# Kernel tuning notes

Hardware: AMD Instinct MI355X
Metric: run time of the kernel (lower is better)

The kernel has to match this reference:

```python
import jax, jax.numpy as jnp
import numpy as np

D_MODEL = 1024
H = 16
D_V = 64
B = 4
N = 1024
LARGE_NEG = -1000000000.0


def setup_inputs() -> dict:
    key = jax.random.key(0)
    k_x, k_q, k_k, k_v, k_o = jax.random.split(key, 5)
    X = jax.random.normal(k_x, (B, N, D_MODEL), dtype=jnp.float32)
    W_q = jax.random.normal(k_q, (H, D_MODEL, D_MODEL), dtype=jnp.float32)
    W_k = jax.random.normal(k_k, (H, D_MODEL, D_MODEL), dtype=jnp.float32)
    W_v = jax.random.normal(k_v, (H, D_MODEL, D_V), dtype=jnp.float32)
    W_o = jax.random.normal(k_o, (H * D_V, D_MODEL), dtype=jnp.float32)
    return {"X": X, "W_q": W_q, "W_k": W_k, "W_v": W_v, "W_o": W_o}


def reference(X, W_q, W_k, W_v, W_o):
    Bb, Nn, Dd = X.shape
    scale = 1.0 / jnp.sqrt(jnp.asarray(Dd, dtype=X.dtype))
    # Per-head projections, batched over heads instead of a Python loop.
    Q = jnp.einsum('bnd,hde->bhne', X, W_q)          # [B,H,N,d_model]
    K = jnp.einsum('bnd,hde->bhne', X, W_k)          # [B,H,N,d_model]
    V = jnp.einsum('bnd,hdv->bhnv', X, W_v)          # [B,H,N,D_v]
    scores = jnp.einsum('bhne,bhme->bhnm', Q, K) * scale  # [B,H,N,N]
    A = jax.nn.softmax(scores, axis=-1)
    Hh = jnp.einsum('bhnm,bhmv->bhnv', A, V)         # [B,H,N,D_v]
    concat = Hh.transpose(0, 2, 1, 3).reshape(Bb, Nn, -1)  # [B,N,H*D_v]
    Y = concat @ W_o                                  # [B,N,d_model]
    # Post-hoc mask: triu over the LAST TWO dims (N, d_model), diagonal=1.
    mask = jnp.triu(jnp.ones((Nn, Dd), dtype=bool), k=1)
    return jnp.where(mask[None, :, :], jnp.asarray(LARGE_NEG, Y.dtype), Y)
```

## Files before the change

kernel.cpp:

```cpp
#include <hip/hip_runtime.h>
#include <stdint.h>

typedef short s16x8 __attribute__((ext_vector_type(8)));
typedef float f32x4 __attribute__((ext_vector_type(4)));

__device__ __forceinline__ unsigned short f2bf(float f) {
  union { float f; unsigned int u; } v; v.f = f;
  unsigned int r = v.u + 0x7FFFu + ((v.u >> 16) & 1u);
  return (unsigned short)(r >> 16);
}

__device__ __forceinline__ unsigned cvt2fp8(float a, float b) {
#if __has_builtin(__builtin_amdgcn_cvt_pk_fp8_f32)
  return (unsigned)__builtin_amdgcn_cvt_pk_fp8_f32(a, b, 0, false);
#else
  unsigned r;
  asm("v_cvt_pk_fp8_f32 %0, %1, %2" : "=v"(r) : "v"(a), "v"(b));
  return r;
#endif
}

__device__ __forceinline__ void gload_lds16(const void* g, void* l) {
  __builtin_amdgcn_global_load_lds(
      (const __attribute__((address_space(1))) unsigned int*)g,
      (__attribute__((address_space(3))) unsigned int*)l, 16, 0, 0);
}

__device__ __forceinline__ unsigned xcd_swz(unsigned fid, unsigned nwg) {
  unsigned cpx = nwg >> 3;
  return (fid & 7) * cpx + (fid >> 3);
}

__global__ void conv_bf16(const float* __restrict__ in, unsigned short* __restrict__ out, int n8) {
  int i = blockIdx.x * blockDim.x + threadIdx.x;
  if (i >= n8) return;
  const f32x4* p = (const f32x4*)(in + (long)i * 8);
  f32x4 a = p[0], b = p[1];
  s16x8 o;
  o[0]=(short)f2bf(a[0]); o[1]=(short)f2bf(a[1]); o[2]=(short)f2bf(a[2]); o[3]=(short)f2bf(a[3]);
  o[4]=(short)f2bf(b[0]); o[5]=(short)f2bf(b[1]); o[6]=(short)f2bf(b[2]); o[7]=(short)f2bf(b[3]);
  *(s16x8*)(out + (long)i * 8) = o;
}

__global__ void conv_x(const float* __restrict__ in, unsigned short* __restrict__ obf,
                       unsigned char* __restrict__ of8, int n8) {
  int i = blockIdx.x * blockDim.x + threadIdx.x;
  if (i >= n8) return;
  const f32x4* p = (const f32x4*)(in + (long)i * 8);
  f32x4 a = p[0], b = p[1];
  s16x8 o;
  o[0]=(short)f2bf(a[0]); o[1]=(short)f2bf(a[1]); o[2]=(short)f2bf(a[2]); o[3]=(short)f2bf(a[3]);
  o[4]=(short)f2bf(b[0]); o[5]=(short)f2bf(b[1]); o[6]=(short)f2bf(b[2]); o[7]=(short)f2bf(b[3]);
  *(s16x8*)(obf + (long)i * 8) = o;
  unsigned long w = (unsigned long)(cvt2fp8(a[0], a[1]) & 0xFFFFu)
                  | ((unsigned long)(cvt2fp8(a[2], a[3]) & 0xFFFFu) << 16)
                  | ((unsigned long)(cvt2fp8(b[0], b[1]) & 0xFFFFu) << 32)
                  | ((unsigned long)(cvt2fp8(b[2], b[3]) & 0xFFFFu) << 48);
  *(unsigned long*)(of8 + (long)i * 8) = w;
}

__global__ void convT_wv(const float* __restrict__ in, unsigned short* __restrict__ out) {
  int i = blockIdx.x * blockDim.x + threadIdx.x;
  int v = i & 63, d = (i >> 6) & 1023, h = i >> 16;
  out[((long)h * 64 + v) * 1024 + d] = f2bf(in[i]);
}

__global__ void convT_wo(const float* __restrict__ in, unsigned short* __restrict__ out) {
  int i = blockIdx.x * blockDim.x + threadIdx.x;
  int e = i & 1023, c = i >> 10;
  out[(long)e * 1024 + c] = f2bf(in[i]);
}

template<int BM, int BN, int WAVES_M, int WAVES_N, int CMODE>
__global__ __launch_bounds__(256, 2)
void gemm_bt(const unsigned short* __restrict__ A, const unsigned short* __restrict__ BT,
             void* __restrict__ Cout, int aDiv, long aStr, int bMod, long bStr,
             long cStr, int ldc)
{
  constexpr int BK = 64;
  constexpr int FM = BM / (WAVES_M * 16);
  constexpr int FN = BN / (WAVES_N * 16);
  __shared__ __align__(16) unsigned short At[BM * BK];
  __shared__ __align__(16) unsigned short Bt[BN * BK];

  unsigned fid = blockIdx.x + gridDim.x * (blockIdx.y + gridDim.y * blockIdx.z);
  unsigned nwg = gridDim.x * gridDim.y * gridDim.z;
  unsigned sid = xcd_swz(fid, nwg);
  unsigned bx = sid % gridDim.x;
  unsigned rem = sid / gridDim.x;
  unsigned by = rem % gridDim.y;
  unsigned bz = rem / gridDim.y;

  const int t = threadIdx.x;
  const int l = t & 63;
  const int g = l >> 4, c = l & 15;
  const int w = t >> 6;
  const int wr = (w / WAVES_N) * (BM / WAVES_M);
  const int wc = (w % WAVES_N) * (BN / WAVES_N);
  const int z = bz;
  const int m0 = by * BM;
  const int n0 = bx * BN;
  const unsigned short* Ab = A + (long)(z / aDiv) * aStr + (long)m0 * 1024;
  const unsigned short* Bb = BT + (long)(z % bMod) * bStr + (long)n0 * 1024;

  const long cbase = (long)z * cStr;

  if constexpr (CMODE == 2) {
    if (n0 > m0 + BM - 1) {
#pragma unroll
      for (int m = 0; m < FM; ++m)
#pragma unroll
        for (int n = 0; n < FN; ++n)
#pragma unroll
          for (int r = 0; r < 4; ++r) {
            int row = wr + m * 16 + g * 4 + r;
            int col = n0 + wc + n * 16 + c;
            ((float*)Cout)[cbase + (long)(m0 + row) * ldc + col] = -1e9f;
          }
      return;
    }
  }

  f32x4 acc[FM][FN] = {};
  constexpr int PA = (BM * BK) / 2048;
  constexpr int PB = (BN * BK) / 2048;

  for (int k0 = 0; k0 < 1024; k0 += BK) {
#pragma unroll
    for (int p = 0; p < PA; ++p) {
      int e = (p * 256 + t) * 8;
      int row = e >> 6, col = e & 63;
      gload_lds16(Ab + (long)row * 1024 + k0 + col, &At[e]);
    }
#pragma unroll
    for (int p = 0; p < PB; ++p) {
      int e = (p * 256 + t) * 8;
      int row = e >> 6, col = e & 63;
      gload_lds16(Bb + (long)row * 1024 + k0 + col, &Bt[e]);
    }
    __syncthreads();
#pragma unroll
    for (int kk = 0; kk < BK; kk += 32) {
      s16x8 af[FM], bf[FN];
#pragma unroll
      for (int m = 0; m < FM; ++m)
        af[m] = *(const s16x8*)&At[(wr + m * 16 + c) * BK + kk + g * 8];
#pragma unroll
      for (int n = 0; n < FN; ++n)
        bf[n] = *(const s16x8*)&Bt[(wc + n * 16 + c) * BK + kk + g * 8];
#pragma unroll
      for (int m = 0; m < FM; ++m)
#pragma unroll
        for (int n = 0; n < FN; ++n)
          acc[m][n] = __builtin_amdgcn_mfma_f32_16x16x32_bf16(af[m], bf[n], acc[m][n], 0, 0, 0);
    }
    __syncthreads();
  }

#pragma unroll
  for (int m = 0; m < FM; ++m)
#pragma unroll
    for (int n = 0; n < FN; ++n) {
      if constexpr (CMODE == 3) {
        int row0 = m0 + wr + m * 16 + g * 4;
        int col  = n0 + wc + n * 16 + c;
        unsigned p01 = cvt2fp8(acc[m][n][0] * 0.00390625f, acc[m][n][1] * 0.00390625f);
        unsigned p23 = cvt2fp8(acc[m][n][2] * 0.00390625f, acc[m][n][3] * 0.00390625f);
        unsigned char* Cp = (unsigned char*)Cout + cbase + (long)row0 * ldc + col;
        Cp[0]            = (unsigned char)p01;
        Cp[(long)ldc]    = (unsigned char)(p01 >> 8);
        Cp[(long)ldc*2]  = (unsigned char)p23;
        Cp[(long)ldc*3]  = (unsigned char)(p23 >> 8);
      } else {
#pragma unroll
        for (int r = 0; r < 4; ++r) {
          int row = wr + m * 16 + g * 4 + r;
          int col = n0 + wc + n * 16 + c;
          int grow = m0 + row;
          float v = acc[m][n][r];
          if constexpr (CMODE == 0) {
            ((unsigned short*)Cout)[cbase + (long)grow * ldc + col] = f2bf(v);
          } else if constexpr (CMODE == 1) {
            ((unsigned short*)Cout)[cbase + (long)col * ldc + grow] = f2bf(v);
          } else if constexpr (CMODE == 2) {
            ((float*)Cout)[cbase + (long)grow * ldc + col] = (col > grow) ? -1e9f : v;
          }
        }
      }
    }
}

__global__ __launch_bounds__(256, 2)
void gemm_f8(const unsigned char* __restrict__ A, const unsigned char* __restrict__ BT,
             unsigned char* __restrict__ Cout)
{
  __shared__ __align__(16) unsigned char At[128 * 128];
  __shared__ __align__(16) unsigned char Bt[128 * 128];

  unsigned fid = blockIdx.x + gridDim.x * (blockIdx.y + gridDim.y * blockIdx.z);
  unsigned nwg = gridDim.x * gridDim.y * gridDim.z;
  unsigned sid = xcd_swz(fid, nwg);
  unsigned bx = sid % gridDim.x;
  unsigned rem = sid / gridDim.x;
  unsigned by = rem % gridDim.y;
  unsigned bz = rem / gridDim.y;

  const int t = threadIdx.x;
  const int l = t & 63;
  const int g = l >> 4, c = l & 15;
  const int w = t >> 6;
  const int wr = (w >> 1) * 64;
  const int wc = (w & 1) * 64;
  const int z = bz;
  const int m0 = by * 128;
  const int n0 = bx * 128;
  const unsigned char* Ab = A + (long)(z >> 4) * (1 << 20) + (long)m0 * 1024;
  const unsigned char* Bb = BT + (long)(z & 15) * (1 << 20) + (long)n0 * 1024;

  f32x4 acc[4][4] = {};

  for (int k0 = 0; k0 < 1024; k0 += 128) {
#pragma unroll
    for (int p = 0; p < 4; ++p) {
      int e = (p * 256 + t) * 16;
      int r = e >> 7, u = (e >> 4) & 7;
      int gcol = ((u ^ (r & 7)) << 4);
      gload_lds16(Ab + (long)r * 1024 + k0 + gcol, &At[e]);
    }
#pragma unroll
    for (int p = 0; p < 4; ++p) {
      int e = (p * 256 + t) * 16;
      int r = e >> 7, u = (e >> 4) & 7;
      int gcol = ((u ^ (r & 7)) << 4);
      gload_lds16(Bb + (long)r * 1024 + k0 + gcol, &Bt[e]);
    }
    __syncthreads();
#pragma unroll
    for (int kk = 0; kk < 128; kk += 32) {
      long af[4], bf[4];
#pragma unroll
      for (int m = 0; m < 4; ++m) {
        int row = wr + m * 16 + c;
        int un = (kk >> 4) + (g >> 1);
        af[m] = *(const long*)&At[row * 128 + ((un ^ (row & 7)) << 4) + (g & 1) * 8];
      }
#pragma unroll
      for (int n = 0; n < 4; ++n) {
        int row = wc + n * 16 + c;
        int un = (kk >> 4) + (g >> 1);
        bf[n] = *(const long*)&Bt[row * 128 + ((un ^ (row & 7)) << 4) + (g & 1) * 8];
      }
      __builtin_amdgcn_s_setprio(1);
#pragma unroll
      for (int m = 0; m < 4; ++m)
#pragma unroll
        for (int n = 0; n < 4; ++n)
          acc[m][n] = __builtin_amdgcn_mfma_f32_16x16x32_fp8_fp8(af[m], bf[n], acc[m][n], 0, 0, 0);
      __builtin_amdgcn_s_setprio(0);
    }
    __syncthreads();
  }

  const long cbase = (long)z << 20;
#pragma unroll
  for (int m = 0; m < 4; ++m)
#pragma unroll
    for (int n = 0; n < 4; ++n) {
      int row0 = m0 + wr + m * 16 + g * 4;
      int col  = n0 + wc + n * 16 + c;
      unsigned p01 = cvt2fp8(acc[m][n][0], acc[m][n][1]);
      unsigned p23 = cvt2fp8(acc[m][n][2], acc[m][n][3]);
      unsigned char* Cp = Cout + cbase + (long)row0 * 1024 + col;
      Cp[0]    = (unsigned char)p01;
      Cp[1024] = (unsigned char)(p01 >> 8);
      Cp[2048] = (unsigned char)p23;
      Cp[3072] = (unsigned char)(p23 >> 8);
    }
}

__global__ __launch_bounds__(256, 2)
void flash_attn(const unsigned char* __restrict__ T, const unsigned char* __restrict__ X,
                const unsigned short* __restrict__ VT, unsigned short* __restrict__ Yc)
{
  __shared__ __align__(16) unsigned char Sh[49152];
  unsigned char* Tt = Sh;
  unsigned char* Xt = Sh + 16384;
  unsigned short* Vt = (unsigned short*)(Sh + 32768);
  unsigned short* Pl = (unsigned short*)Sh;

  unsigned fid = blockIdx.x + gridDim.x * blockIdx.y;
  unsigned nwg = gridDim.x * gridDim.y;
  unsigned sid = xcd_swz(fid, nwg);
  const int q0 = (sid % gridDim.x) * 128;
  const int bh = sid / gridDim.x;

  const int t = threadIdx.x;
  const int l = t & 63;
  const int w = t >> 6;
  const int g = l >> 4;
  const int c = l & 15;
  const int b = bh >> 4;

  const unsigned char* Tq = T + (long)bh * (1024 * 1024) + (long)q0 * 1024;
  const unsigned char* Xb = X + (long)b * (1024 * 1024);
  const unsigned short* Vb = VT + (long)bh * (64 * 1024);

  f32x4 accO[2][4] = {};
  float mrun[2][4], lrun[2][4];
#pragma unroll
  for (int m = 0; m < 2; ++m)
#pragma unroll
    for (int r = 0; r < 4; ++r) { mrun[m][r] = -1e30f; lrun[m][r] = 0.f; }

  const float scale = 8.0f;

  for (int m0 = 0; m0 < 1024; m0 += 128) {
    f32x4 accS[2][8] = {};
    for (int k0 = 0; k0 < 1024; k0 += 128) {
#pragma unroll
      for (int p = 0; p < 4; ++p) {
        int e = (p * 256 + t) * 16;
        int r = e >> 7, u = (e >> 4) & 7;
        int gcol = ((u ^ (r & 7)) << 4);
        gload_lds16(Tq + (long)r * 1024 + k0 + gcol, &Tt[e]);
      }
#pragma unroll
      for (int p = 0; p < 4; ++p) {
        int e = (p * 256 + t) * 16;
        int r = e >> 7, u = (e >> 4) & 7;
        int gcol = ((u ^ (r & 7)) << 4);
        gload_lds16(Xb + (long)(m0 + r) * 1024 + k0 + gcol, &Xt[e]);
      }
      __syncthreads();
#pragma unroll
      for (int kk = 0; kk < 128; kk += 32) {
        long af[2], bf[8];
#pragma unroll
        for (int m = 0; m < 2; ++m) {
          int row = w * 32 + m * 16 + c;
          int un = (kk >> 4) + (g >> 1);
          af[m] = *(const long*)&Tt[row * 128 + ((un ^ (row & 7)) << 4) + (g & 1) * 8];
        }
#pragma unroll
        for (int n = 0; n < 8; ++n) {
          int row = n * 16 + c;
          int un = (kk >> 4) + (g >> 1);
          bf[n] = *(const long*)&Xt[row * 128 + ((un ^ (row & 7)) << 4) + (g & 1) * 8];
        }
        __builtin_amdgcn_s_setprio(1);
#pragma unroll
        for (int m = 0; m < 2; ++m)
#pragma unroll
          for (int n = 0; n < 8; ++n)
            accS[m][n] = __builtin_amdgcn_mfma_f32_16x16x32_fp8_fp8(af[m], bf[n], accS[m][n], 0, 0, 0);
        __builtin_amdgcn_s_setprio(0);
      }
      __syncthreads();
    }
#pragma unroll
    for (int p = 0; p < 4; ++p) {
      int e = (p * 256 + t) * 8;
      int r = e >> 7, u = (e >> 3) & 15;
      int gcol = ((u ^ (r & 7)) << 3);
      gload_lds16(Vb + (long)r * 1024 + m0 + gcol, &Vt[e]);
    }
    float alpha[2][4];
#pragma unroll
    for (int m = 0; m < 2; ++m) {
#pragma unroll
      for (int r = 0; r < 4; ++r) {
        float mx = -1e30f;
#pragma unroll
        for (int n = 0; n < 8; ++n) mx = fmaxf(mx, accS[m][n][r]);
#pragma unroll
        for (int s = 1; s < 16; s <<= 1) mx = fmaxf(mx, __shfl_xor(mx, s));
        mx *= scale;
        float mnew = fmaxf(mrun[m][r], mx);
        float a = __expf(mrun[m][r] - mnew);
        alpha[m][r] = a;
        float sum = 0.f;
#pragma unroll
        for (int n = 0; n < 8; ++n) {
          float pe = __expf(accS[m][n][r] * scale - mnew);
          accS[m][n][r] = pe;
          sum += pe;
        }
#pragma unroll
        for (int s = 1; s < 16; s <<= 1) sum += __shfl_xor(sum, s);
        lrun[m][r] = lrun[m][r] * a + sum;
        mrun[m][r] = mnew;
      }
    }
#pragma unroll
    for (int m = 0; m < 2; ++m)
#pragma unroll
      for (int n = 0; n < 8; ++n)
#pragma unroll
        for (int r = 0; r < 4; ++r) {
          int row = w * 32 + m * 16 + g * 4 + r;
          int un = 2 * n + (c >> 3);
          Pl[row * 128 + ((un ^ (row & 7)) << 3) + (c & 7)] = f2bf(accS[m][n][r]);
        }
    __syncthreads();
#pragma unroll
    for (int m = 0; m < 2; ++m)
#pragma unroll
      for (int n = 0; n < 4; ++n)
#pragma unroll
        for (int r = 0; r < 4; ++r)
          accO[m][n][r] *= alpha[m][r];
#pragma unroll
    for (int kk = 0; kk < 128; kk += 32) {
      s16x8 pa[2], vb[4];
#pragma unroll
      for (int m = 0; m < 2; ++m) {
        int row = w * 32 + m * 16 + c;
        int un = (kk >> 3) + g;
        pa[m] = *(const s16x8*)&Pl[row * 128 + ((un ^ (row & 7)) << 3)];
      }
#pragma unroll
      for (int n = 0; n < 4; ++n) {
        int row = n * 16 + c;
        int un = (kk >> 3) + g;
        vb[n] = *(const s16x8*)&Vt[row * 128 + ((un ^ (row & 7)) << 3)];
      }
      __builtin_amdgcn_s_setprio(1);
#pragma unroll
      for (int m = 0; m < 2; ++m)
#pragma unroll
        for (int n = 0; n < 4; ++n)
          accO[m][n] = __builtin_amdgcn_mfma_f32_16x16x32_bf16(pa[m], vb[n], accO[m][n], 0, 0, 0);
      __builtin_amdgcn_s_setprio(0);
    }
    __syncthreads();
  }
  unsigned short* out = Yc + (long)b * (1024 * 1024) + (long)(bh & 15) * 64;
#pragma unroll
  for (int m = 0; m < 2; ++m)
#pragma unroll
    for (int n = 0; n < 4; ++n)
#pragma unroll
      for (int r = 0; r < 4; ++r) {
        int row = q0 + w * 32 + m * 16 + g * 4 + r;
        int col = n * 16 + c;
        out[(long)row * 1024 + col] = f2bf(accO[m][n][r] / lrun[m][r]);
      }
}

extern "C" void kernel_launch(void* const* d_in, const int* in_sizes, int n_in,
                              void* d_out, int out_size, void* d_ws, size_t ws_size,
                              hipStream_t stream) {
  (void)in_sizes; (void)n_in; (void)out_size; (void)ws_size;
  const float* X  = (const float*)d_in[0];
  const float* Wq = (const float*)d_in[1];
  const float* Wk = (const float*)d_in[2];
  const float* Wv = (const float*)d_in[3];
  const float* Wo = (const float*)d_in[4];
  float* Y = (float*)d_out;
  char* ws = (char*)d_ws;

  const long MB = 1L << 20;
  unsigned short* Xbf  = (unsigned short*)(ws + 0);
  unsigned short* Wqb  = (unsigned short*)(ws + 8  * MB);
  unsigned short* Wkb  = (unsigned short*)(ws + 40 * MB);
  unsigned char*  Mtf8 = (unsigned char*)(ws + 72 * MB);
  unsigned char*  Tf8  = (unsigned char*)(ws + 104 * MB);
  unsigned char*  Xf8  = (unsigned char*)(ws + 168 * MB);
  unsigned short* WvT  = (unsigned short*)(ws + 8  * MB);
  unsigned short* VTb  = (unsigned short*)(ws + 10 * MB);
  unsigned short* Ccat = (unsigned short*)(ws + 18 * MB);
  unsigned short* WoT  = (unsigned short*)(ws + 26 * MB);

  const long M1 = 1L << 20;

  conv_x   <<<2048, 256, 0, stream>>>(X,  Xbf, Xf8, 524288);
  conv_bf16<<<8192, 256, 0, stream>>>(Wq, Wqb, 2097152);
  conv_bf16<<<8192, 256, 0, stream>>>(Wk, Wkb, 2097152);

  gemm_bt<128, 128, 2, 2, 3><<<dim3(8, 8, 16), 256, 0, stream>>>(
      Wkb, Wqb, Mtf8, 1, M1, 16, M1, M1, 1024);

  gemm_f8<<<dim3(8, 8, 64), 256, 0, stream>>>(Xf8, Mtf8, Tf8);

  convT_wv<<<4096, 256, 0, stream>>>(Wv, WvT);
  gemm_bt<128, 64, 4, 1, 1><<<dim3(1, 8, 64), 256, 0, stream>>>(
      Xbf, WvT, VTb, 16, M1, 16, 65536, 65536, 1024);

  flash_attn<<<dim3(8, 64), 256, 0, stream>>>(Tf8, Xf8, VTb, Ccat);

  convT_wo<<<4096, 256, 0, stream>>>(Wo, WoT);
  gemm_bt<128, 128, 2, 2, 2><<<dim3(8, 8, 4), 256, 0, stream>>>(
      Ccat, WoT, Y, 1, M1, 1, 0, M1, 1024);
}
```

Measured before the change: 389.5 us.

## Double-buffer LDS tiles in fp8 GEMM and flash-attention score loops

Both the fp8 projection GEMM and the QK score loop in flash attention now use two LDS stages. The global-to-LDS loads for the next k-tile are issued before the MFMA work on the current tile, with explicit vmcnt waits and raw s_barrier calls in place of __syncthreads. The aim is to hide global load latency behind compute instead of stalling at each tile. In exchange, LDS per block grows to 64KB for the GEMM and 80KB for attention, which at two blocks per CU may limit occupancy.

Measured after the change: 403.6 us. +3.6%, slower.

```diff
diff --git a/kernel.cpp b/kernel.cpp
--- a/kernel.cpp
+++ b/kernel.cpp
@@ -194,8 +194,7 @@
 void gemm_f8(const unsigned char* __restrict__ A, const unsigned char* __restrict__ BT,
              unsigned char* __restrict__ Cout)
 {
-  __shared__ __align__(16) unsigned char At[128 * 128];
-  __shared__ __align__(16) unsigned char Bt[128 * 128];
+  __shared__ __align__(16) unsigned char Sh[65536];
 
   unsigned fid = blockIdx.x + gridDim.x * (blockIdx.y + gridDim.y * blockIdx.z);
   unsigned nwg = gridDim.x * gridDim.y * gridDim.z;
@@ -219,22 +218,51 @@
 
   f32x4 acc[4][4] = {};
 
-  for (int k0 = 0; k0 < 1024; k0 += 128) {
-#pragma unroll
-    for (int p = 0; p < 4; ++p) {
-      int e = (p * 256 + t) * 16;
-      int r = e >> 7, u = (e >> 4) & 7;
-      int gcol = ((u ^ (r & 7)) << 4);
-      gload_lds16(Ab + (long)r * 1024 + k0 + gcol, &At[e]);
-    }
-#pragma unroll
-    for (int p = 0; p < 4; ++p) {
-      int e = (p * 256 + t) * 16;
-      int r = e >> 7, u = (e >> 4) & 7;
-      int gcol = ((u ^ (r & 7)) << 4);
-      gload_lds16(Bb + (long)r * 1024 + k0 + gcol, &Bt[e]);
-    }
-    __syncthreads();
+#pragma unroll
+  for (int p = 0; p < 4; ++p) {
+    int e = (p * 256 + t) * 16;
+    int r = e >> 7, u = (e >> 4) & 7;
+    int gcol = ((u ^ (r & 7)) << 4);
+    gload_lds16(Ab + (long)r * 1024 + 0 + gcol, &Sh[e]);
+  }
+#pragma unroll
+  for (int p = 0; p < 4; ++p) {
+    int e = (p * 256 + t) * 16;
+    int r = e >> 7, u = (e >> 4) & 7;
+    int gcol = ((u ^ (r & 7)) << 4);
+    gload_lds16(Bb + (long)r * 1024 + 0 + gcol, &Sh[16384 + e]);
+  }
+
+  int cur = 0;
+  for (int it = 0; it < 8; ++it) {
+    int k0 = it << 7;
+    if (it < 7) {
+      unsigned char* Ad = Sh + (cur ^ 1) * 32768;
+      unsigned char* Bd = Ad + 16384;
+#pragma unroll
+      for (int p = 0; p < 4; ++p) {
+        int e = (p * 256 + t) * 16;
+        int r = e >> 7, u = (e >> 4) & 7;
+        int gcol = ((u ^ (r & 7)) << 4);
+        gload_lds16(Ab + (long)r * 1024 + (k0 + 128) + gcol, &Ad[e]);
+      }
+#pragma unroll
+      for (int p = 0; p < 4; ++p) {
+        int e = (p * 256 + t) * 16;
+        int r = e >> 7, u = (e >> 4) & 7;
+        int gcol = ((u ^ (r & 7)) << 4);
+        gload_lds16(Bb + (long)r * 1024 + (k0 + 128) + gcol, &Bd[e]);
+      }
+      asm volatile("s_waitcnt vmcnt(8)" ::: "memory");
+    } else {
+      asm volatile("s_waitcnt vmcnt(0)" ::: "memory");
+    }
+    __builtin_amdgcn_sched_barrier(0);
+    __builtin_amdgcn_s_barrier();
+    __builtin_amdgcn_sched_barrier(0);
+
+    const unsigned char* At = Sh + cur * 32768;
+    const unsigned char* Bt = At + 16384;
 #pragma unroll
     for (int kk = 0; kk < 128; kk += 32) {
       long af[4], bf[4];
@@ -258,7 +286,10 @@
           acc[m][n] = __builtin_amdgcn_mfma_f32_16x16x32_fp8_fp8(af[m], bf[n], acc[m][n], 0, 0, 0);
       __builtin_amdgcn_s_setprio(0);
     }
-    __syncthreads();
+    __builtin_amdgcn_sched_barrier(0);
+    __builtin_amdgcn_s_barrier();
+    __builtin_amdgcn_sched_barrier(0);
+    cur ^= 1;
   }
 
   const long cbase = (long)z << 20;
@@ -282,10 +313,8 @@
 void flash_attn(const unsigned char* __restrict__ T, const unsigned char* __restrict__ X,
                 const unsigned short* __restrict__ VT, unsigned short* __restrict__ Yc)
 {
-  __shared__ __align__(16) unsigned char Sh[49152];
-  unsigned char* Tt = Sh;
-  unsigned char* Xt = Sh + 16384;
-  unsigned short* Vt = (unsigned short*)(Sh + 32768);
+  __shared__ __align__(16) unsigned char Sh[81920];
+  unsigned short* Vt = (unsigned short*)(Sh + 65536);
   unsigned short* Pl = (unsigned short*)Sh;
 
   unsigned fid = blockIdx.x + gridDim.x * blockIdx.y;
@@ -316,22 +345,50 @@
 
   for (int m0 = 0; m0 < 1024; m0 += 128) {
     f32x4 accS[2][8] = {};
-    for (int k0 = 0; k0 < 1024; k0 += 128) {
-#pragma unroll
-      for (int p = 0; p < 4; ++p) {
-        int e = (p * 256 + t) * 16;
-        int r = e >> 7, u = (e >> 4) & 7;
-        int gcol = ((u ^ (r & 7)) << 4);
-        gload_lds16(Tq + (long)r * 1024 + k0 + gcol, &Tt[e]);
-      }
-#pragma unroll
-      for (int p = 0; p < 4; ++p) {
-        int e = (p * 256 + t) * 16;
-        int r = e >> 7, u = (e >> 4) & 7;
-        int gcol = ((u ^ (r & 7)) << 4);
-        gload_lds16(Xb + (long)(m0 + r) * 1024 + k0 + gcol, &Xt[e]);
-      }
-      __syncthreads();
+#pragma unroll
+    for (int p = 0; p < 4; ++p) {
+      int e = (p * 256 + t) * 16;
+      int r = e >> 7, u = (e >> 4) & 7;
+      int gcol = ((u ^ (r & 7)) << 4);
+      gload_lds16(Tq + (long)r * 1024 + 0 + gcol, &Sh[e]);
+    }
+#pragma unroll
+    for (int p = 0; p < 4; ++p) {
+      int e = (p * 256 + t) * 16;
+      int r = e >> 7, u = (e >> 4) & 7;
+      int gcol = ((u ^ (r & 7)) << 4);
+      gload_lds16(Xb + (long)(m0 + r) * 1024 + 0 + gcol, &Sh[16384 + e]);
+    }
+    int cur = 0;
+    for (int it = 0; it < 8; ++it) {
+      int k0 = it << 7;
+      if (it < 7) {
+        unsigned char* Td = Sh + (cur ^ 1) * 32768;
+        unsigned char* Xd = Td + 16384;
+#pragma unroll
+        for (int p = 0; p < 4; ++p) {
+          int e = (p * 256 + t) * 16;
+          int r = e >> 7, u = (e >> 4) & 7;
+          int gcol = ((u ^ (r & 7)) << 4);
+          gload_lds16(Tq + (long)r * 1024 + (k0 + 128) + gcol, &Td[e]);
+        }
+#pragma unroll
+        for (int p = 0; p < 4; ++p) {
+          int e = (p * 256 + t) * 16;
+          int r = e >> 7, u = (e >> 4) & 7;
+          int gcol = ((u ^ (r & 7)) << 4);
+          gload_lds16(Xb + (long)(m0 + r) * 1024 + (k0 + 128) + gcol, &Xd[e]);
+        }
+        asm volatile("s_waitcnt vmcnt(8)" ::: "memory");
+      } else {
+        asm volatile("s_waitcnt vmcnt(0)" ::: "memory");
+      }
+      __builtin_amdgcn_sched_barrier(0);
+      __builtin_amdgcn_s_barrier();
+      __builtin_amdgcn_sched_barrier(0);
+
+      const unsigned char* Tt = Sh + cur * 32768;
+      const unsigned char* Xt = Tt + 16384;
 #pragma unroll
       for (int kk = 0; kk < 128; kk += 32) {
         long af[2], bf[8];
@@ -355,7 +412,10 @@
             accS[m][n] = __builtin_amdgcn_mfma_f32_16x16x32_fp8_fp8(af[m], bf[n], accS[m][n], 0, 0, 0);
         __builtin_amdgcn_s_setprio(0);
       }
-      __syncthreads();
+      __builtin_amdgcn_sched_barrier(0);
+      __builtin_amdgcn_s_barrier();
+      __builtin_amdgcn_sched_barrier(0);
+      cur ^= 1;
     }
 #pragma unroll
     for (int p = 0; p < 4; ++p) {
```

## Move Wk·Wq, V projection and PV matmul from bf16 to fp8

Applied to the files above, without the earlier changes.

Converts Wq, Wk, Wv and X to fp8 only, dropping the bf16 copies. The Wk·Wq product and the V projection now run through a generalized templated fp8 GEMM, and the V projection output is stored transposed. Inside flash attention, P and V are kept as fp8 in LDS and the PV product uses the fp8 MFMA. The aim is to halve conversion and weight traffic and use the faster fp8 MFMA, at the cost of more precision loss in the weights, V and probabilities.

Result: faster. 346.6 us (-11.0%).

```diff
diff --git a/kernel.cpp b/kernel.cpp
--- a/kernel.cpp
+++ b/kernel.cpp
@@ -31,38 +31,22 @@
   return (fid & 7) * cpx + (fid >> 3);
 }
 
-__global__ void conv_bf16(const float* __restrict__ in, unsigned short* __restrict__ out, int n8) {
+__global__ void conv_fp8(const float* __restrict__ in, unsigned char* __restrict__ out, int n8) {
   int i = blockIdx.x * blockDim.x + threadIdx.x;
   if (i >= n8) return;
   const f32x4* p = (const f32x4*)(in + (long)i * 8);
   f32x4 a = p[0], b = p[1];
-  s16x8 o;
-  o[0]=(short)f2bf(a[0]); o[1]=(short)f2bf(a[1]); o[2]=(short)f2bf(a[2]); o[3]=(short)f2bf(a[3]);
-  o[4]=(short)f2bf(b[0]); o[5]=(short)f2bf(b[1]); o[6]=(short)f2bf(b[2]); o[7]=(short)f2bf(b[3]);
-  *(s16x8*)(out + (long)i * 8) = o;
-}
-
-__global__ void conv_x(const float* __restrict__ in, unsigned short* __restrict__ obf,
-                       unsigned char* __restrict__ of8, int n8) {
-  int i = blockIdx.x * blockDim.x + threadIdx.x;
-  if (i >= n8) return;
-  const f32x4* p = (const f32x4*)(in + (long)i * 8);
-  f32x4 a = p[0], b = p[1];
-  s16x8 o;
-  o[0]=(short)f2bf(a[0]); o[1]=(short)f2bf(a[1]); o[2]=(short)f2bf(a[2]); o[3]=(short)f2bf(a[3]);
-  o[4]=(short)f2bf(b[0]); o[5]=(short)f2bf(b[1]); o[6]=(short)f2bf(b[2]); o[7]=(short)f2bf(b[3]);
-  *(s16x8*)(obf + (long)i * 8) = o;
   unsigned long w = (unsigned long)(cvt2fp8(a[0], a[1]) & 0xFFFFu)
                   | ((unsigned long)(cvt2fp8(a[2], a[3]) & 0xFFFFu) << 16)
                   | ((unsigned long)(cvt2fp8(b[0], b[1]) & 0xFFFFu) << 32)
                   | ((unsigned long)(cvt2fp8(b[2], b[3]) & 0xFFFFu) << 48);
-  *(unsigned long*)(of8 + (long)i * 8) = w;
-}
-
-__global__ void convT_wv(const float* __restrict__ in, unsigned short* __restrict__ out) {
+  *(unsigned long*)(out + (long)i * 8) = w;
+}
+
+__global__ void convT_wv_f8(const float* __restrict__ in, unsigned char* __restrict__ out) {
   int i = blockIdx.x * blockDim.x + threadIdx.x;
   int v = i & 63, d = (i >> 6) & 1023, h = i >> 16;
-  out[((long)h * 64 + v) * 1024 + d] = f2bf(in[i]);
+  out[((long)h * 64 + v) * 1024 + d] = (unsigned char)cvt2fp8(in[i], 0.f);
 }
 
 __global__ void convT_wo(const float* __restrict__ in, unsigned short* __restrict__ out) {
@@ -160,42 +144,31 @@
 #pragma unroll
   for (int m = 0; m < FM; ++m)
 #pragma unroll
-    for (int n = 0; n < FN; ++n) {
-      if constexpr (CMODE == 3) {
-        int row0 = m0 + wr + m * 16 + g * 4;
-        int col  = n0 + wc + n * 16 + c;
-        unsigned p01 = cvt2fp8(acc[m][n][0] * 0.00390625f, acc[m][n][1] * 0.00390625f);
-        unsigned p23 = cvt2fp8(acc[m][n][2] * 0.00390625f, acc[m][n][3] * 0.00390625f);
-        unsigned char* Cp = (unsigned char*)Cout + cbase + (long)row0 * ldc + col;
-        Cp[0]            = (unsigned char)p01;
-        Cp[(long)ldc]    = (unsigned char)(p01 >> 8);
-        Cp[(long)ldc*2]  = (unsigned char)p23;
-        Cp[(long)ldc*3]  = (unsigned char)(p23 >> 8);
-      } else {
-#pragma unroll
-        for (int r = 0; r < 4; ++r) {
-          int row = wr + m * 16 + g * 4 + r;
-          int col = n0 + wc + n * 16 + c;
-          int grow = m0 + row;
-          float v = acc[m][n][r];
-          if constexpr (CMODE == 0) {
-            ((unsigned short*)Cout)[cbase + (long)grow * ldc + col] = f2bf(v);
-          } else if constexpr (CMODE == 1) {
-            ((unsigned short*)Cout)[cbase + (long)col * ldc + grow] = f2bf(v);
-          } else if constexpr (CMODE == 2) {
-            ((float*)Cout)[cbase + (long)grow * ldc + col] = (col > grow) ? -1e9f : v;
-          }
+    for (int n = 0; n < FN; ++n)
+#pragma unroll
+      for (int r = 0; r < 4; ++r) {
+        int row = wr + m * 16 + g * 4 + r;
+        int col = n0 + wc + n * 16 + c;
+        int grow = m0 + row;
+        float v = acc[m][n][r];
+        if constexpr (CMODE == 0) {
+          ((unsigned short*)Cout)[cbase + (long)grow * ldc + col] = f2bf(v);
+        } else if constexpr (CMODE == 2) {
+          ((float*)Cout)[cbase + (long)grow * ldc + col] = (col > grow) ? -1e9f : v;
         }
       }
-    }
-}
-
+}
+
+template<int BM, int BN, int WM, int WN, int TRANS>
 __global__ __launch_bounds__(256, 2)
 void gemm_f8(const unsigned char* __restrict__ A, const unsigned char* __restrict__ BT,
-             unsigned char* __restrict__ Cout)
+             unsigned char* __restrict__ Cout, int aDiv, long aStr, int bMod, long bStr,
+             long cStr, int ldc, float scale)
 {
-  __shared__ __align__(16) unsigned char At[128 * 128];
-  __shared__ __align__(16) unsigned char Bt[128 * 128];
+  constexpr int FM = BM / (WM * 16);
+  constexpr int FN = BN / (WN * 16);
+  __shared__ __align__(16) unsigned char At[BM * 128];
+  __shared__ __align__(16) unsigned char Bt[BN * 128];
 
   unsigned fid = blockIdx.x + gridDim.x * (blockIdx.y + gridDim.y * blockIdx.z);
   unsigned nwg = gridDim.x * gridDim.y * gridDim.z;
@@ -209,26 +182,28 @@
   const int l = t & 63;
   const int g = l >> 4, c = l & 15;
   const int w = t >> 6;
-  const int wr = (w >> 1) * 64;
-  const int wc = (w & 1) * 64;
+  const int wr = (w / WN) * (BM / WM);
+  const int wc = (w % WN) * (BN / WN);
   const int z = bz;
-  const int m0 = by * 128;
-  const int n0 = bx * 128;
-  const unsigned char* Ab = A + (long)(z >> 4) * (1 << 20) + (long)m0 * 1024;
-  const unsigned char* Bb = BT + (long)(z & 15) * (1 << 20) + (long)n0 * 1024;
-
-  f32x4 acc[4][4] = {};
+  const int m0 = by * BM;
+  const int n0 = bx * BN;
+  const unsigned char* Ab = A + (long)(z / aDiv) * aStr + (long)m0 * 1024;
+  const unsigned char* Bb = BT + (long)(z % bMod) * bStr + (long)n0 * 1024;
+
+  f32x4 acc[FM][FN] = {};
+  constexpr int PA = (BM * 128) / (256 * 16);
+  constexpr int PB = (BN * 128) / (256 * 16);
 
   for (int k0 = 0; k0 < 1024; k0 += 128) {
 #pragma unroll
-    for (int p = 0; p < 4; ++p) {
+    for (int p = 0; p < PA; ++p) {
       int e = (p * 256 + t) * 16;
       int r = e >> 7, u = (e >> 4) & 7;
       int gcol = ((u ^ (r & 7)) << 4);
       gload_lds16(Ab + (long)r * 1024 + k0 + gcol, &At[e]);
     }
 #pragma unroll
-    for (int p = 0; p < 4; ++p) {
+    for (int p = 0; p < PB; ++p) {
       int e = (p * 256 + t) * 16;
       int r = e >> 7, u = (e >> 4) & 7;
       int gcol = ((u ^ (r & 7)) << 4);
@@ -237,56 +212,61 @@
     __syncthreads();
 #pragma unroll
     for (int kk = 0; kk < 128; kk += 32) {
-      long af[4], bf[4];
-#pragma unroll
-      for (int m = 0; m < 4; ++m) {
+      long af[FM], bf[FN];
+#pragma unroll
+      for (int m = 0; m < FM; ++m) {
         int row = wr + m * 16 + c;
         int un = (kk >> 4) + (g >> 1);
         af[m] = *(const long*)&At[row * 128 + ((un ^ (row & 7)) << 4) + (g & 1) * 8];
       }
 #pragma unroll
-      for (int n = 0; n < 4; ++n) {
+      for (int n = 0; n < FN; ++n) {
         int row = wc + n * 16 + c;
         int un = (kk >> 4) + (g >> 1);
         bf[n] = *(const long*)&Bt[row * 128 + ((un ^ (row & 7)) << 4) + (g & 1) * 8];
       }
       __builtin_amdgcn_s_setprio(1);
 #pragma unroll
-      for (int m = 0; m < 4; ++m)
-#pragma unroll
-        for (int n = 0; n < 4; ++n)
+      for (int m = 0; m < FM; ++m)
+#pragma unroll
+        for (int n = 0; n < FN; ++n)
           acc[m][n] = __builtin_amdgcn_mfma_f32_16x16x32_fp8_fp8(af[m], bf[n], acc[m][n], 0, 0, 0);
       __builtin_amdgcn_s_setprio(0);
     }
     __syncthreads();
   }
 
-  const long cbase = (long)z << 20;
-#pragma unroll
-  for (int m = 0; m < 4; ++m)
-#pragma unroll
-    for (int n = 0; n < 4; ++n) {
+  const long cbase = (long)z * cStr;
+#pragma unroll
+  for (int m = 0; m < FM; ++m)
+#pragma unroll
+    for (int n = 0; n < FN; ++n) {
       int row0 = m0 + wr + m * 16 + g * 4;
       int col  = n0 + wc + n * 16 + c;
-      unsigned p01 = cvt2fp8(acc[m][n][0], acc[m][n][1]);
-      unsigned p23 = cvt2fp8(acc[m][n][2], acc[m][n][3]);
-      unsigned char* Cp = Cout + cbase + (long)row0 * 1024 + col;
-      Cp[0]    = (unsigned char)p01;
-      Cp[1024] = (unsigned char)(p01 >> 8);
-      Cp[2048] = (unsigned char)p23;
-      Cp[3072] = (unsigned char)(p23 >> 8);
+      unsigned p01 = cvt2fp8(acc[m][n][0] * scale, acc[m][n][1] * scale);
+      unsigned p23 = cvt2fp8(acc[m][n][2] * scale, acc[m][n][3] * scale);
+      if constexpr (TRANS == 0) {
+        unsigned char* Cp = Cout + cbase + (long)row0 * ldc + col;
+        Cp[0]            = (unsigned char)p01;
+        Cp[(long)ldc]    = (unsigned char)(p01 >> 8);
+        Cp[(long)ldc*2]  = (unsigned char)p23;
+        Cp[(long)ldc*3]  = (unsigned char)(p23 >> 8);
+      } else {
+        unsigned word = (p01 & 0xFFFFu) | (p23 << 16);
+        *(unsigned*)(Cout + cbase + (long)col * ldc + row0) = word;
+      }
     }
 }
 
 __global__ __launch_bounds__(256, 2)
 void flash_attn(const unsigned char* __restrict__ T, const unsigned char* __restrict__ X,
-                const unsigned short* __restrict__ VT, unsigned short* __restrict__ Yc)
+                const unsigned char* __restrict__ VT, unsigned short* __restrict__ Yc)
 {
-  __shared__ __align__(16) unsigned char Sh[49152];
-  unsigned char* Tt = Sh;
-  unsigned char* Xt = Sh + 16384;
-  unsigned short* Vt = (unsigned short*)(Sh + 32768);
-  unsigned short* Pl = (unsigned short*)Sh;
+  __shared__ __align__(16) unsigned char Sh[40960];
+  unsigned char* Tt  = Sh;
+  unsigned char* Xt  = Sh + 16384;
+  unsigned char* Vt8 = Sh + 32768;
+  unsigned char* Pl8 = Sh;
 
   unsigned fid = blockIdx.x + gridDim.x * blockIdx.y;
   unsigned nwg = gridDim.x * gridDim.y;
@@ -303,7 +283,7 @@
 
   const unsigned char* Tq = T + (long)bh * (1024 * 1024) + (long)q0 * 1024;
   const unsigned char* Xb = X + (long)b * (1024 * 1024);
-  const unsigned short* Vb = VT + (long)bh * (64 * 1024);
+  const unsigned char* Vb = VT + (long)bh * (64 * 1024);
 
   f32x4 accO[2][4] = {};
   float mrun[2][4], lrun[2][4];
@@ -358,11 +338,11 @@
       __syncthreads();
     }
 #pragma unroll
-    for (int p = 0; p < 4; ++p) {
-      int e = (p * 256 + t) * 8;
-      int r = e >> 7, u = (e >> 3) & 15;
-      int gcol = ((u ^ (r & 7)) << 3);
-      gload_lds16(Vb + (long)r * 1024 + m0 + gcol, &Vt[e]);
+    for (int p = 0; p < 2; ++p) {
+      int e = (p * 256 + t) * 16;
+      int r = e >> 7, u = (e >> 4) & 7;
+      int gcol = ((u ^ (r & 7)) << 4);
+      gload_lds16(Vb + (long)r * 1024 + m0 + gcol, &Vt8[e]);
     }
     float alpha[2][4];
 #pragma unroll
@@ -398,8 +378,8 @@
 #pragma unroll
         for (int r = 0; r < 4; ++r) {
           int row = w * 32 + m * 16 + g * 4 + r;
-          int un = 2 * n + (c >> 3);
-          Pl[row * 128 + ((un ^ (row & 7)) << 3) + (c & 7)] = f2bf(accS[m][n][r]);
+          Pl8[row * 128 + ((n ^ (row & 7)) << 4) + c] =
+              (unsigned char)cvt2fp8(accS[m][n][r], 0.f);
         }
     __syncthreads();
 #pragma unroll
@@ -411,25 +391,25 @@
           accO[m][n][r] *= alpha[m][r];
 #pragma unroll
     for (int kk = 0; kk < 128; kk += 32) {
-      s16x8 pa[2], vb[4];
+      long pa[2], vb[4];
 #pragma unroll
       for (int m = 0; m < 2; ++m) {
         int row = w * 32 + m * 16 + c;
-        int un = (kk >> 3) + g;
-        pa[m] = *(const s16x8*)&Pl[row * 128 + ((un ^ (row & 7)) << 3)];
+        int un = (kk >> 4) + (g >> 1);
+        pa[m] = *(const long*)&Pl8[row * 128 + ((un ^ (row & 7)) << 4) + (g & 1) * 8];
       }
 #pragma unroll
       for (int n = 0; n < 4; ++n) {
         int row = n * 16 + c;
-        int un = (kk >> 3) + g;
-        vb[n] = *(const s16x8*)&Vt[row * 128 + ((un ^ (row & 7)) << 3)];
+        int un = (kk >> 4) + (g >> 1);
+        vb[n] = *(const long*)&Vt8[row * 128 + ((un ^ (row & 7)) << 4) + (g & 1) * 8];
       }
       __builtin_amdgcn_s_setprio(1);
 #pragma unroll
       for (int m = 0; m < 2; ++m)
 #pragma unroll
         for (int n = 0; n < 4; ++n)
-          accO[m][n] = __builtin_amdgcn_mfma_f32_16x16x32_bf16(pa[m], vb[n], accO[m][n], 0, 0, 0);
+          accO[m][n] = __builtin_amdgcn_mfma_f32_16x16x32_fp8_fp8(pa[m], vb[n], accO[m][n], 0, 0, 0);
       __builtin_amdgcn_s_setprio(0);
     }
     __syncthreads();
@@ -460,33 +440,33 @@
   char* ws = (char*)d_ws;
 
   const long MB = 1L << 20;
-  unsigned short* Xbf  = (unsigned short*)(ws + 0);
-  unsigned short* Wqb  = (unsigned short*)(ws + 8  * MB);
-  unsigned short* Wkb  = (unsigned short*)(ws + 40 * MB);
-  unsigned char*  Mtf8 = (unsigned char*)(ws + 72 * MB);
-  unsigned char*  Tf8  = (unsigned char*)(ws + 104 * MB);
-  unsigned char*  Xf8  = (unsigned char*)(ws + 168 * MB);
-  unsigned short* WvT  = (unsigned short*)(ws + 8  * MB);
-  unsigned short* VTb  = (unsigned short*)(ws + 10 * MB);
-  unsigned short* Ccat = (unsigned short*)(ws + 18 * MB);
-  unsigned short* WoT  = (unsigned short*)(ws + 26 * MB);
+  unsigned char*  Xf8   = (unsigned char*)(ws + 0);
+  unsigned char*  Wqf8  = (unsigned char*)(ws + 4  * MB);
+  unsigned char*  Wkf8  = (unsigned char*)(ws + 20 * MB);
+  unsigned char*  Mtf8  = (unsigned char*)(ws + 36 * MB);
+  unsigned char*  WvTf8 = (unsigned char*)(ws + 52 * MB);
+  unsigned char*  VTb8  = (unsigned char*)(ws + 56 * MB);
+  unsigned short* Ccat  = (unsigned short*)(ws + 60 * MB);
+  unsigned short* WoT   = (unsigned short*)(ws + 68 * MB);
+  unsigned char*  Tf8   = (unsigned char*)(ws + 72 * MB);
 
   const long M1 = 1L << 20;
 
-  conv_x   <<<2048, 256, 0, stream>>>(X,  Xbf, Xf8, 524288);
-  conv_bf16<<<8192, 256, 0, stream>>>(Wq, Wqb, 2097152);
-  conv_bf16<<<8192, 256, 0, stream>>>(Wk, Wkb, 2097152);
-
-  gemm_bt<128, 128, 2, 2, 3><<<dim3(8, 8, 16), 256, 0, stream>>>(
-      Wkb, Wqb, Mtf8, 1, M1, 16, M1, M1, 1024);
-
-  gemm_f8<<<dim3(8, 8, 64), 256, 0, stream>>>(Xf8, Mtf8, Tf8);
-
-  convT_wv<<<4096, 256, 0, stream>>>(Wv, WvT);
-  gemm_bt<128, 64, 4, 1, 1><<<dim3(1, 8, 64), 256, 0, stream>>>(
-      Xbf, WvT, VTb, 16, M1, 16, 65536, 65536, 1024);
-
-  flash_attn<<<dim3(8, 64), 256, 0, stream>>>(Tf8, Xf8, VTb, Ccat);
+  conv_fp8<<<2048, 256, 0, stream>>>(X,  Xf8,  524288);
+  conv_fp8<<<8192, 256, 0, stream>>>(Wq, Wqf8, 2097152);
+  conv_fp8<<<8192, 256, 0, stream>>>(Wk, Wkf8, 2097152);
+  convT_wv_f8<<<4096, 256, 0, stream>>>(Wv, WvTf8);
+
+  gemm_f8<128, 128, 2, 2, 0><<<dim3(8, 8, 16), 256, 0, stream>>>(
+      Wkf8, Wqf8, Mtf8, 1, M1, 16, M1, M1, 1024, 0.00390625f);
+
+  gemm_f8<128, 128, 2, 2, 0><<<dim3(8, 8, 64), 256, 0, stream>>>(
+      Xf8, Mtf8, Tf8, 16, M1, 16, M1, M1, 1024, 1.0f);
+
+  gemm_f8<128, 64, 4, 1, 1><<<dim3(1, 8, 64), 256, 0, stream>>>(
+      Xf8, WvTf8, VTb8, 16, M1, 16, 65536, 65536, 1024, 1.0f);
+
+  flash_attn<<<dim3(8, 64), 256, 0, stream>>>(Tf8, Xf8, VTb8, Ccat);
 
   convT_wo<<<4096, 256, 0, stream>>>(Wo, WoT);
   gemm_bt<128, 128, 2, 2, 2><<<dim3(8, 8, 4), 256, 0, stream>>>(
```
